# Kernel tuning notes

Measured on AMD Instinct MI355X. Metric: run time of the kernel, lower is better.

## Reference

```python
import jax, jax.numpy as jnp
import numpy as np

N_DRUG = 572
EMB = 256
K_NB = 128
N_TAIL = 100000
N_REL = 200
N_EDGE = 4576
BN_EPS = 1e-5


def setup_inputs() -> dict:
    key = jax.random.key(0)
    ks = jax.random.split(key, 12)
    return {
        "drug_name": jnp.arange(N_DRUG, dtype=jnp.int64 if jax.config.jax_enable_x64 else jnp.int32),
        "adj_tail": jax.random.randint(ks[0], (N_DRUG, K_NB), 0, N_TAIL),
        "adj_relation": jax.random.randint(ks[1], (N_DRUG, K_NB), 0, N_REL),
        "nb_src": jax.random.randint(ks[2], (N_EDGE,), 0, N_DRUG),
        "nb_dst": jax.random.randint(ks[3], (N_EDGE,), 0, N_DRUG),
        "epoch": 2,
        # learned parameters
        "drug_table": jax.random.normal(ks[4], (N_DRUG, EMB), dtype=jnp.float32),
        "rela_table": jax.random.normal(ks[5], (N_REL, EMB), dtype=jnp.float32),
        "ent_table": jax.random.normal(ks[6], (N_TAIL, EMB), dtype=jnp.float32),
        "lin_W": jax.random.normal(ks[7], (2 * EMB, EMB), dtype=jnp.float32) * (1.0 / np.sqrt(2 * EMB)),
        "lin_b": jnp.zeros((EMB,), dtype=jnp.float32),
        "bn_gamma": jnp.ones((EMB,), dtype=jnp.float32),
        "bn_beta": jnp.zeros((EMB,), dtype=jnp.float32),
    }


def reference(drug_name, adj_tail, adj_relation, nb_src, nb_dst, epoch,
              drug_table, rela_table, ent_table, lin_W, lin_b, bn_gamma, bn_beta):
    # --- embedding gathers ---
    d = drug_table[drug_name]          # [N, E]
    r = rela_table[adj_relation]       # [N, K, E]
    e = ent_table[adj_tail]            # [N, K, E]

    # --- attention over sampled neighbors (KGNN-style: score = <drug, relation>) ---
    scores = jnp.einsum('ne,nke->nk', d, r)              # [N, K]
    alpha = jax.nn.softmax(scores, axis=1)               # softmax over neighbors
    attended = jnp.einsum('nk,nke->ne', alpha, e)        # [N, E]

    # --- Linear(2E -> E) + ReLU + BatchNorm1d (training-mode batch stats) ---
    x = jnp.concatenate([attended, d], axis=1)           # [N, 2E]
    h = jax.nn.relu(x @ lin_W + lin_b)                   # [N, E]
    mean = jnp.mean(h, axis=0)
    var = jnp.mean((h - mean) ** 2, axis=0)              # biased var, as in torch BN
    drug_f = (h - mean) * jax.lax.rsqrt(var + BN_EPS) * bn_gamma + bn_beta

    # --- invariant-adjacency segment-average scatter update (epoch > 1) ---
    if epoch > 1:
        nb_sum = jax.ops.segment_sum(drug_f[nb_src], nb_dst, num_segments=N_DRUG)   # [N, E]
        cnt = jax.ops.segment_sum(jnp.ones_like(nb_dst, dtype=drug_f.dtype), nb_dst,
                                  num_segments=N_DRUG)                               # [N]
        nb_avg = nb_sum / jnp.maximum(cnt, 1.0)[:, None]
        drug_f = jnp.where((cnt > 0)[:, None], (nb_avg + drug_f) * 0.5, drug_f)
    return drug_f
```

## Files before the change

kernel.cpp:

```cpp
#include <hip/hip_runtime.h>

#define N_DRUG 572
#define EMB    256
#define K_NB   128
#define N_REL  200
#define N_TAIL 100000
#define N_EDGE 4576
#define BN_EPS 1e-5f

__global__ __launch_bounds__(256) void attn_kernel(
    const int* __restrict__ drug_name,
    const int* __restrict__ adj_tail,
    const int* __restrict__ adj_relation,
    const float* __restrict__ drug_table,
    const float* __restrict__ rela_table,
    const float* __restrict__ ent_table,
    float* __restrict__ x)
{
    __shared__ float ld[EMB];
    __shared__ float sc[K_NB];
    __shared__ int   tails[K_NB];
    __shared__ float wred[2];

    const int b    = blockIdx.x;
    const int tid  = threadIdx.x;
    const int lane = tid & 63;
    const int wv   = tid >> 6;

    const int didx = drug_name[b];
    ld[tid] = drug_table[(size_t)didx * EMB + tid];
    if (tid < K_NB) tails[tid] = adj_tail[b * K_NB + tid];
    __syncthreads();

    for (int k = wv; k < K_NB; k += 4) {
        const int rel = adj_relation[b * K_NB + k];
        const float* rr = rela_table + (size_t)rel * EMB;
        float p = 0.f;
        #pragma unroll
        for (int j = 0; j < 4; ++j) {
            const int e = lane + 64 * j;
            p = fmaf(ld[e], rr[e], p);
        }
        #pragma unroll
        for (int off = 32; off > 0; off >>= 1)
            p += __shfl_xor(p, off, 64);
        if (lane == 0) sc[k] = p;
    }
    __syncthreads();

    float pv = 0.f;
    if (tid < K_NB) {
        float m = sc[tid];
        #pragma unroll
        for (int off = 32; off > 0; off >>= 1)
            m = fmaxf(m, __shfl_xor(m, off, 64));
        if (lane == 0) wred[wv] = m;
    }
    __syncthreads();
    if (tid < K_NB) {
        const float m = fmaxf(wred[0], wred[1]);
        pv = __expf(sc[tid] - m);
        float s = pv;
        #pragma unroll
        for (int off = 32; off > 0; off >>= 1)
            s += __shfl_xor(s, off, 64);
        if (lane == 0) wred[wv] = s;
    }
    __syncthreads();
    float tot;
    if (tid < K_NB) tot = wred[0] + wred[1];
    __syncthreads();
    if (tid < K_NB) sc[tid] = pv / tot;
    __syncthreads();

    float acc = 0.f;
    #pragma unroll 4
    for (int k = 0; k < K_NB; ++k) {
        acc = fmaf(sc[k], ent_table[(size_t)tails[k] * EMB + tid], acc);
    }
    x[(size_t)b * (2 * EMB) + tid]       = acc;
    x[(size_t)b * (2 * EMB) + EMB + tid] = ld[tid];
}

#define RPB 8
__global__ __launch_bounds__(256) void linear_kernel(
    const float* __restrict__ x,
    const float* __restrict__ W,
    const float* __restrict__ bias,
    float* __restrict__ h,
    float* __restrict__ s1,
    float* __restrict__ s2)
{
    __shared__ float lx[RPB][2 * EMB];
    const int b0  = blockIdx.x * RPB;
    const int tid = threadIdx.x;

    for (int i = tid; i < RPB * 2 * EMB; i += 256) {
        const int r = i >> 9, c = i & 511;
        const int row = b0 + r;
        lx[r][c] = (row < N_DRUG) ? x[(size_t)row * (2 * EMB) + c] : 0.f;
    }
    __syncthreads();

    float acc[RPB];
    #pragma unroll
    for (int r = 0; r < RPB; ++r) acc[r] = 0.f;

    for (int i = 0; i < 2 * EMB; ++i) {
        const float w = W[(size_t)i * EMB + tid];
        #pragma unroll
        for (int r = 0; r < RPB; ++r)
            acc[r] = fmaf(lx[r][i], w, acc[r]);
    }

    const float bb = bias[tid];
    float lsum = 0.f, lsq = 0.f;
    #pragma unroll
    for (int r = 0; r < RPB; ++r) {
        const int row = b0 + r;
        if (row < N_DRUG) {
            const float v = fmaxf(acc[r] + bb, 0.f);
            h[(size_t)row * EMB + tid] = v;
            lsum += v;
            lsq  = fmaf(v, v, lsq);
        }
    }
    atomicAdd(&s1[tid], lsum);
    atomicAdd(&s2[tid], lsq);
}

__global__ __launch_bounds__(256) void bn_kernel(
    const float* __restrict__ h,
    const float* __restrict__ s1, const float* __restrict__ s2,
    const float* __restrict__ gamma, const float* __restrict__ beta,
    float* __restrict__ f)
{
    const int col = threadIdx.x;
    const size_t idx = (size_t)blockIdx.x * EMB + col;
    const float invN = 1.0f / (float)N_DRUG;
    const float mean = s1[col] * invN;
    const float var  = s2[col] * invN - mean * mean;
    const float scale = gamma[col] * rsqrtf(var + BN_EPS);
    f[idx] = (h[idx] - mean) * scale + beta[col];
}

#define EPB 16
__global__ __launch_bounds__(256) void scatter_kernel(
    const int* __restrict__ nb_src, const int* __restrict__ nb_dst,
    const int* __restrict__ epoch,
    const float* __restrict__ f,
    float* __restrict__ nb_sum,
    float* __restrict__ cnt)
{
    if (*epoch <= 1) return;
    const int tid = threadIdx.x;
    const int e0  = blockIdx.x * EPB;
    const int e1  = min(e0 + EPB, N_EDGE);
    for (int e = e0; e < e1; ++e) {
        const int s = nb_src[e];
        const int d = nb_dst[e];
        atomicAdd(&nb_sum[(size_t)d * EMB + tid], f[(size_t)s * EMB + tid]);
        if (tid == 0) atomicAdd(&cnt[d], 1.0f);
    }
}

__global__ __launch_bounds__(256) void combine_kernel(
    const float* __restrict__ f,
    const float* __restrict__ nb_sum,
    const float* __restrict__ cnt,
    const int* __restrict__ epoch,
    float* __restrict__ out)
{
    const int b = blockIdx.x;
    const size_t idx = (size_t)b * EMB + threadIdx.x;
    float v = f[idx];
    if (*epoch > 1) {
        const float c = cnt[b];
        if (c > 0.f) v = (nb_sum[idx] / c + v) * 0.5f;
    }
    out[idx] = v;
}

extern "C" void kernel_launch(void* const* d_in, const int* in_sizes, int n_in,
                              void* d_out, int out_size, void* d_ws, size_t ws_size,
                              hipStream_t stream) {
    const int*   drug_name    = (const int*)d_in[0];
    const int*   adj_tail     = (const int*)d_in[1];
    const int*   adj_relation = (const int*)d_in[2];
    const int*   nb_src       = (const int*)d_in[3];
    const int*   nb_dst       = (const int*)d_in[4];
    const int*   epoch        = (const int*)d_in[5];
    const float* drug_table   = (const float*)d_in[6];
    const float* rela_table   = (const float*)d_in[7];
    const float* ent_table    = (const float*)d_in[8];
    const float* lin_W        = (const float*)d_in[9];
    const float* lin_b        = (const float*)d_in[10];
    const float* bn_gamma     = (const float*)d_in[11];
    const float* bn_beta      = (const float*)d_in[12];
    float* out = (float*)d_out;

    float* ws = (float*)d_ws;
    float* x      = ws;
    float* h      = x + N_DRUG * 2 * EMB;
    float* f      = h + N_DRUG * EMB;
    float* s1     = f + N_DRUG * EMB;
    float* s2     = s1 + EMB;
    float* cnt    = s2 + EMB;
    float* nb_sum = cnt + N_DRUG;
    const size_t zero_bytes = (size_t)(EMB + EMB + N_DRUG + N_DRUG * EMB) * sizeof(float);

    hipMemsetAsync(s1, 0, zero_bytes, stream);

    attn_kernel<<<N_DRUG, 256, 0, stream>>>(drug_name, adj_tail, adj_relation,
                                            drug_table, rela_table, ent_table, x);

    linear_kernel<<<(N_DRUG + RPB - 1) / RPB, 256, 0, stream>>>(x, lin_W, lin_b, h, s1, s2);

    bn_kernel<<<N_DRUG, 256, 0, stream>>>(h, s1, s2, bn_gamma, bn_beta, f);

    scatter_kernel<<<(N_EDGE + EPB - 1) / EPB, 256, 0, stream>>>(nb_src, nb_dst, epoch,
                                                                 f, nb_sum, cnt);

    combine_kernel<<<N_DRUG, 256, 0, stream>>>(f, nb_sum, cnt, epoch, out);
}
```

Baseline: 247.5 us.

## Fuse attention with linear layer and fold batchnorm into scatter and combine

Merges the attention kernel with the per-row linear+ReLU so the concatenated input stays in shared memory, and removes the separate BN pass by recomputing normalization inside the scatter and combine kernels. Relation and entity gathers are vectorized to float4, with the neighbor sum split across four waves and reduced through shared memory. The linear stage now reads the full weight matrix once per drug row instead of once per eight rows, which raises L2 traffic for W. It also issues one atomic per row for the BN statistics instead of one per eight rows. EPB is halved to 8.

```diff
diff --git a/kernel.cpp b/kernel.cpp
--- a/kernel.cpp
+++ b/kernel.cpp
@@ -3,23 +3,27 @@
 #define N_DRUG 572
 #define EMB    256
 #define K_NB   128
-#define N_REL  200
-#define N_TAIL 100000
 #define N_EDGE 4576
 #define BN_EPS 1e-5f
 
-__global__ __launch_bounds__(256) void attn_kernel(
+__global__ __launch_bounds__(256) void fused_attn_lin(
     const int* __restrict__ drug_name,
     const int* __restrict__ adj_tail,
     const int* __restrict__ adj_relation,
     const float* __restrict__ drug_table,
     const float* __restrict__ rela_table,
     const float* __restrict__ ent_table,
-    float* __restrict__ x)
+    const float* __restrict__ lin_W,
+    const float* __restrict__ lin_b,
+    float* __restrict__ h,
+    float* __restrict__ s1,
+    float* __restrict__ s2)
 {
-    __shared__ float ld[EMB];
+    __shared__ float xs[2 * EMB];
     __shared__ float sc[K_NB];
     __shared__ int   tails[K_NB];
+    __shared__ int   rels[K_NB];
+    __shared__ float part[4][EMB];
     __shared__ float wred[2];
 
     const int b    = blockIdx.x;
@@ -28,19 +32,17 @@
     const int wv   = tid >> 6;
 
     const int didx = drug_name[b];
-    ld[tid] = drug_table[(size_t)didx * EMB + tid];
-    if (tid < K_NB) tails[tid] = adj_tail[b * K_NB + tid];
+    xs[EMB + tid] = drug_table[(size_t)didx * EMB + tid];
+    if (tid < K_NB) {
+        tails[tid] = adj_tail[b * K_NB + tid];
+        rels[tid]  = adj_relation[b * K_NB + tid];
+    }
     __syncthreads();
 
+    const float4 dv = ((const float4*)(xs + EMB))[lane];
     for (int k = wv; k < K_NB; k += 4) {
-        const int rel = adj_relation[b * K_NB + k];
-        const float* rr = rela_table + (size_t)rel * EMB;
-        float p = 0.f;
-        #pragma unroll
-        for (int j = 0; j < 4; ++j) {
-            const int e = lane + 64 * j;
-            p = fmaf(ld[e], rr[e], p);
-        }
+        const float4 rv = ((const float4*)(rela_table + (size_t)rels[k] * EMB))[lane];
+        float p = dv.x * rv.x + dv.y * rv.y + dv.z * rv.z + dv.w * rv.w;
         #pragma unroll
         for (int off = 32; off > 0; off >>= 1)
             p += __shfl_xor(p, off, 64);
@@ -67,118 +69,90 @@
         if (lane == 0) wred[wv] = s;
     }
     __syncthreads();
-    float tot;
-    if (tid < K_NB) tot = wred[0] + wred[1];
-    __syncthreads();
-    if (tid < K_NB) sc[tid] = pv / tot;
-    __syncthreads();
-
-    float acc = 0.f;
-    #pragma unroll 4
-    for (int k = 0; k < K_NB; ++k) {
-        acc = fmaf(sc[k], ent_table[(size_t)tails[k] * EMB + tid], acc);
-    }
-    x[(size_t)b * (2 * EMB) + tid]       = acc;
-    x[(size_t)b * (2 * EMB) + EMB + tid] = ld[tid];
-}
-
-#define RPB 8
-__global__ __launch_bounds__(256) void linear_kernel(
-    const float* __restrict__ x,
-    const float* __restrict__ W,
-    const float* __restrict__ bias,
-    float* __restrict__ h,
-    float* __restrict__ s1,
-    float* __restrict__ s2)
-{
-    __shared__ float lx[RPB][2 * EMB];
-    const int b0  = blockIdx.x * RPB;
-    const int tid = threadIdx.x;
-
-    for (int i = tid; i < RPB * 2 * EMB; i += 256) {
-        const int r = i >> 9, c = i & 511;
-        const int row = b0 + r;
-        lx[r][c] = (row < N_DRUG) ? x[(size_t)row * (2 * EMB) + c] : 0.f;
+    if (tid < K_NB) {
+        const float tot = wred[0] + wred[1];
+        sc[tid] = pv / tot;
     }
     __syncthreads();
 
-    float acc[RPB];
-    #pragma unroll
-    for (int r = 0; r < RPB; ++r) acc[r] = 0.f;
+    float4 acc = make_float4(0.f, 0.f, 0.f, 0.f);
+    #pragma unroll 8
+    for (int kk = 0; kk < 32; ++kk) {
+        const int k = wv * 32 + kk;
+        const float a = sc[k];
+        const float4 ev = ((const float4*)(ent_table + (size_t)tails[k] * EMB))[lane];
+        acc.x = fmaf(a, ev.x, acc.x);
+        acc.y = fmaf(a, ev.y, acc.y);
+        acc.z = fmaf(a, ev.z, acc.z);
+        acc.w = fmaf(a, ev.w, acc.w);
+    }
+    ((float4*)part[wv])[lane] = acc;
+    __syncthreads();
+    xs[tid] = part[0][tid] + part[1][tid] + part[2][tid] + part[3][tid];
+    __syncthreads();
 
-    for (int i = 0; i < 2 * EMB; ++i) {
-        const float w = W[(size_t)i * EMB + tid];
-        #pragma unroll
-        for (int r = 0; r < RPB; ++r)
-            acc[r] = fmaf(lx[r][i], w, acc[r]);
-    }
+    float accL = 0.f;
+    #pragma unroll 8
+    for (int i = 0; i < 2 * EMB; ++i)
+        accL = fmaf(xs[i], lin_W[(size_t)i * EMB + tid], accL);
 
-    const float bb = bias[tid];
-    float lsum = 0.f, lsq = 0.f;
-    #pragma unroll
-    for (int r = 0; r < RPB; ++r) {
-        const int row = b0 + r;
-        if (row < N_DRUG) {
-            const float v = fmaxf(acc[r] + bb, 0.f);
-            h[(size_t)row * EMB + tid] = v;
-            lsum += v;
-            lsq  = fmaf(v, v, lsq);
-        }
-    }
-    atomicAdd(&s1[tid], lsum);
-    atomicAdd(&s2[tid], lsq);
+    const float v = fmaxf(accL + lin_b[tid], 0.f);
+    h[(size_t)b * EMB + tid] = v;
+    atomicAdd(&s1[tid], v);
+    atomicAdd(&s2[tid], v * v);
 }
 
-__global__ __launch_bounds__(256) void bn_kernel(
+#define EPB 8
+__global__ __launch_bounds__(256) void scatter_bn(
+    const int* __restrict__ nb_src, const int* __restrict__ nb_dst,
+    const int* __restrict__ epoch,
     const float* __restrict__ h,
     const float* __restrict__ s1, const float* __restrict__ s2,
     const float* __restrict__ gamma, const float* __restrict__ beta,
-    float* __restrict__ f)
-{
-    const int col = threadIdx.x;
-    const size_t idx = (size_t)blockIdx.x * EMB + col;
-    const float invN = 1.0f / (float)N_DRUG;
-    const float mean = s1[col] * invN;
-    const float var  = s2[col] * invN - mean * mean;
-    const float scale = gamma[col] * rsqrtf(var + BN_EPS);
-    f[idx] = (h[idx] - mean) * scale + beta[col];
-}
-
-#define EPB 16
-__global__ __launch_bounds__(256) void scatter_kernel(
-    const int* __restrict__ nb_src, const int* __restrict__ nb_dst,
-    const int* __restrict__ epoch,
-    const float* __restrict__ f,
     float* __restrict__ nb_sum,
     float* __restrict__ cnt)
 {
     if (*epoch <= 1) return;
     const int tid = threadIdx.x;
-    const int e0  = blockIdx.x * EPB;
-    const int e1  = min(e0 + EPB, N_EDGE);
+    const float invN  = 1.0f / (float)N_DRUG;
+    const float mean  = s1[tid] * invN;
+    const float var   = s2[tid] * invN - mean * mean;
+    const float scale = gamma[tid] * rsqrtf(var + BN_EPS);
+    const float bet   = beta[tid];
+
+    const int e0 = blockIdx.x * EPB;
+    const int e1 = min(e0 + EPB, N_EDGE);
     for (int e = e0; e < e1; ++e) {
         const int s = nb_src[e];
         const int d = nb_dst[e];
-        atomicAdd(&nb_sum[(size_t)d * EMB + tid], f[(size_t)s * EMB + tid]);
+        const float f = (h[(size_t)s * EMB + tid] - mean) * scale + bet;
+        atomicAdd(&nb_sum[(size_t)d * EMB + tid], f);
         if (tid == 0) atomicAdd(&cnt[d], 1.0f);
     }
 }
 
-__global__ __launch_bounds__(256) void combine_kernel(
-    const float* __restrict__ f,
+__global__ __launch_bounds__(256) void combine_bn(
+    const float* __restrict__ h,
+    const float* __restrict__ s1, const float* __restrict__ s2,
+    const float* __restrict__ gamma, const float* __restrict__ beta,
     const float* __restrict__ nb_sum,
     const float* __restrict__ cnt,
     const int* __restrict__ epoch,
     float* __restrict__ out)
 {
-    const int b = blockIdx.x;
-    const size_t idx = (size_t)b * EMB + threadIdx.x;
-    float v = f[idx];
+    const int b   = blockIdx.x;
+    const int tid = threadIdx.x;
+    const size_t idx = (size_t)b * EMB + tid;
+    const float invN  = 1.0f / (float)N_DRUG;
+    const float mean  = s1[tid] * invN;
+    const float var   = s2[tid] * invN - mean * mean;
+    const float scale = gamma[tid] * rsqrtf(var + BN_EPS);
+    float f = (h[idx] - mean) * scale + beta[tid];
     if (*epoch > 1) {
         const float c = cnt[b];
-        if (c > 0.f) v = (nb_sum[idx] / c + v) * 0.5f;
+        if (c > 0.f) f = (nb_sum[idx] / c + f) * 0.5f;
     }
-    out[idx] = v;
+    out[idx] = f;
 }
 
 extern "C" void kernel_launch(void* const* d_in, const int* in_sizes, int n_in,
@@ -200,10 +174,8 @@
     float* out = (float*)d_out;
 
     float* ws = (float*)d_ws;
-    float* x      = ws;
-    float* h      = x + N_DRUG * 2 * EMB;
-    float* f      = h + N_DRUG * EMB;
-    float* s1     = f + N_DRUG * EMB;
+    float* h      = ws;
+    float* s1     = h + N_DRUG * EMB;
     float* s2     = s1 + EMB;
     float* cnt    = s2 + EMB;
     float* nb_sum = cnt + N_DRUG;
@@ -211,15 +183,14 @@
 
     hipMemsetAsync(s1, 0, zero_bytes, stream);
 
-    attn_kernel<<<N_DRUG, 256, 0, stream>>>(drug_name, adj_tail, adj_relation,
-                                            drug_table, rela_table, ent_table, x);
+    fused_attn_lin<<<N_DRUG, 256, 0, stream>>>(drug_name, adj_tail, adj_relation,
+                                               drug_table, rela_table, ent_table,
+                                               lin_W, lin_b, h, s1, s2);
 
-    linear_kernel<<<(N_DRUG + RPB - 1) / RPB, 256, 0, stream>>>(x, lin_W, lin_b, h, s1, s2);
+    scatter_bn<<<(N_EDGE + EPB - 1) / EPB, 256, 0, stream>>>(nb_src, nb_dst, epoch,
+                                                             h, s1, s2, bn_gamma, bn_beta,
+                                                             nb_sum, cnt);
 
-    bn_kernel<<<N_DRUG, 256, 0, stream>>>(h, s1, s2, bn_gamma, bn_beta, f);
-
-    scatter_kernel<<<(N_EDGE + EPB - 1) / EPB, 256, 0, stream>>>(nb_src, nb_dst, epoch,
-                                                                 f, nb_sum, cnt);
-
-    combine_kernel<<<N_DRUG, 256, 0, stream>>>(f, nb_sum, cnt, epoch, out);
+    combine_bn<<<N_DRUG, 256, 0, stream>>>(h, s1, s2, bn_gamma, bn_beta,
+                                           nb_sum, cnt, epoch, out);
 }
```

After: 233.8 us. 1.06x faster.
